# Kernel optimization log

Hardware: AMD Instinct MI355X
Metric: run time of the kernel (lower is better)

Reference implementation:

```python
import jax, jax.numpy as jnp
import numpy as np

N = 300_000      # active voxels
L = 128          # occupied bounding grid side
M = 32           # unet width m
CIN = 3          # input_feature_number
NCLASS = 20
K = 27           # 3x3x3 submanifold kernel
BLOCK_REPS = 2
BN_EPS = 1e-4


def _build_neighbors(rng):
    """Rulebook: for each active voxel, index of each of its 27 neighbors (N = missing)."""
    coords = rng.integers(0, L, size=(int(N * 1.5), 3), dtype=np.int64)
    keys = coords[:, 0] * L * L + coords[:, 1] * L + coords[:, 2]
    keys = np.unique(keys)[:N]
    assert keys.shape[0] == N
    x = keys // (L * L); y = (keys // L) % L; z = keys % L
    c = np.stack([x, y, z], 1)                      # [N,3] sorted-by-key coords
    nbr = np.full((N, K), N, dtype=np.int32)
    k = 0
    for dx in (-1, 0, 1):
        for dy in (-1, 0, 1):
            for dz in (-1, 0, 1):
                nc = c + np.array([dx, dy, dz])
                valid = ((nc >= 0) & (nc < L)).all(1)
                nk = nc[:, 0] * L * L + nc[:, 1] * L + nc[:, 2]
                pos = np.searchsorted(keys, nk).clip(0, N - 1)
                found = valid & (keys[pos] == nk)
                nbr[:, k] = np.where(found, pos, N).astype(np.int32)
                k += 1
    return nbr


def setup_inputs() -> dict:
    rng = np.random.default_rng(0)
    nbr_idx = jnp.asarray(_build_neighbors(rng))
    key = jax.random.key(0)
    ks = jax.random.split(key, 16)
    s = 0.1
    inp = {
        "features": jax.random.normal(ks[0], (N, CIN), jnp.float32),
        "nbr_idx": nbr_idx,
        # initial SubmanifoldConvolution(3, m, 3, bias=False)
        "w0": jax.random.normal(ks[1], (K, CIN, M), jnp.float32) * s,
        # residual tower params: [rep, conv_in_block(2), ...]
        "bw": jax.random.normal(ks[2], (BLOCK_REPS, 2, K, M, M), jnp.float32) * s,
        "bg": jnp.ones((BLOCK_REPS, 2, M), jnp.float32),
        "bb": jnp.zeros((BLOCK_REPS, 2, M), jnp.float32),
        # final BatchNormReLU(m)
        "gf": jnp.ones((M,), jnp.float32),
        "bf": jnp.zeros((M,), jnp.float32),
        # dense heads
        "w_cls": jax.random.normal(ks[3], (M, NCLASS), jnp.float32) * s,
        "b_cls": jnp.zeros((NCLASS,), jnp.float32),
        "w_fe": jax.random.normal(ks[4], (M, M), jnp.float32) * s,
        "b_fe": jnp.zeros((M,), jnp.float32),
        "w_le": jax.random.normal(ks[5], (M, M), jnp.float32) * s,
        "b_le": jnp.zeros((M,), jnp.float32),
        "w_fr": jax.random.normal(ks[6], (M, M), jnp.float32) * s,
        "b_fr": jnp.zeros((M,), jnp.float32),
        "w_lr": jax.random.normal(ks[7], (M, 1), jnp.float32) * s,
        "b_lr": jnp.zeros((1,), jnp.float32),
    }
    return inp


def _subconv(feat, nbr, W):
    # feat [N,Cin], nbr [N,27] with sentinel N -> zero row, W [27,Cin,Cout]
    fpad = jnp.concatenate([feat, jnp.zeros((1, feat.shape[1]), feat.dtype)], 0)
    gathered = fpad[nbr]                       # [N,27,Cin] irregular gather
    return jnp.einsum('nkc,kcd->nd', gathered, W)


def _bn(x, g, b):
    mu = x.mean(0)
    var = ((x - mu) ** 2).mean(0)
    return (x - mu) * jax.lax.rsqrt(var + BN_EPS) * g + b


def reference(features, nbr_idx, w0, bw, bg, bb, gf, bf,
              w_cls, b_cls, w_fe, b_fe, w_le, b_le, w_fr, b_fr, w_lr, b_lr):
    feat = _subconv(features, nbr_idx, w0)     # [N,M]
    for r in range(BLOCK_REPS):                # pre-activation residual blocks
        h = _subconv(jax.nn.relu(_bn(feat, bg[r, 0], bb[r, 0])), nbr_idx, bw[r, 0])
        h = _subconv(jax.nn.relu(_bn(h, bg[r, 1], bb[r, 1])), nbr_idx, bw[r, 1])
        feat = feat + h
    feat = jax.nn.relu(_bn(feat, gf, bf))      # BatchNormReLU(m) + OutputLayer
    y = feat @ w_cls + b_cls                                   # [N,20]
    embedding = (feat @ w_fe + b_fe) @ w_le + b_le             # [N,32]
    offset = jax.nn.sigmoid((feat @ w_fr + b_fr) @ w_lr + b_lr)  # [N,1]
    return (y, embedding, offset)
```

## Files before the change

### kernel.cpp

```cpp
#include <hip/hip_runtime.h>

#define NVOX 300000
#define K27 27
#define VPB 128
#define TILES 2
#define NBLK 2344
#define CPX  (NBLK/8)

typedef __attribute__((ext_vector_type(8))) __bf16 bf16x8;
typedef __attribute__((ext_vector_type(8))) unsigned short ushort8;
typedef __attribute__((ext_vector_type(4))) float f32x4;

__device__ inline unsigned short f2bf(float x){
  unsigned int u = __float_as_uint(x);
  unsigned int r = (u + 0x7FFFu + ((u >> 16) & 1u)) >> 16;
  return (unsigned short)r;
}

__global__ void pack_w_kernel(const float* __restrict__ bw, const float* __restrict__ w0,
                              unsigned short* __restrict__ pw, unsigned short* __restrict__ pw0){
  int t = blockIdx.x*256 + threadIdx.x;
  if (t < 4*K27*2*64){
    int l  = t & 63;
    int h  = (t >> 6) & 1;
    int k  = (t >> 7) % K27;
    int cv = t / (128*K27);
    int g = l >> 4, r16 = l & 15;
    ushort8 o;
    #pragma unroll
    for (int i = 0; i < 8; ++i){
      int c  = g*8 + i;
      int oc = h*16 + r16;
      o[i] = f2bf(bw[(((cv*K27 + k)*32) + c)*32 + oc]);
    }
    *reinterpret_cast<ushort8*>(pw + t*8) = o;
    return;
  }
  int u = t - 4*K27*2*64;
  if (u >= 4*2*64) return;
  int l  = u & 63;
  int h  = (u >> 6) & 1;
  int kb = u >> 7;
  int g = l >> 4, r16 = l & 15;
  int col = h*16 + r16;
  ushort8 o;
  #pragma unroll
  for (int i = 0; i < 8; ++i){
    int k   = kb*32 + g*8 + i;
    int tap = k >> 2, ch = k & 3;
    float v = (tap < K27 && ch < 3) ? w0[(tap*3 + ch)*32 + col] : 0.f;
    o[i] = f2bf(v);
  }
  *reinterpret_cast<ushort8*>(pw0 + u*8) = o;
}

__global__ void pack_hw_kernel(const float* __restrict__ w_cls, const float* __restrict__ b_cls,
                               const float* __restrict__ w_fe,  const float* __restrict__ b_fe,
                               const float* __restrict__ w_le,
                               const float* __restrict__ w_fr,  const float* __restrict__ b_fr,
                               unsigned short* __restrict__ pwh, float* __restrict__ bcat){
  int t = blockIdx.x*512 + threadIdx.x;
  if (t < 96){
    float v = 0.f;
    if (t < 32)      v = b_fe[t];
    else if (t < 64) v = b_fr[t-32];
    else if (t < 84) v = b_cls[t-64];
    bcat[t] = v;
  }
  if (t >= 8*64) return;
  int l = t & 63, f = t >> 6;
  int g = l >> 4, r16 = l & 15;
  ushort8 o;
  #pragma unroll
  for (int i = 0; i < 8; ++i){
    int k = g*8 + i;
    float v;
    if (f < 6){
      int col = f*16 + r16;
      if (col < 32)      v = w_fe[k*32 + col];
      else if (col < 64) v = w_fr[k*32 + (col-32)];
      else { int c = col - 64; v = (c < 20) ? w_cls[k*20 + c] : 0.f; }
    } else {
      int col = (f-6)*16 + r16;
      v = w_le[k*32 + col];
    }
    o[i] = f2bf(v);
  }
  *reinterpret_cast<ushort8*>(pwh + t*8) = o;
}

__global__ void prepad_kernel(const float* __restrict__ feats, f32x4* __restrict__ fpad){
  int row = blockIdx.x*256 + threadIdx.x;
  if (row > NVOX) return;
  f32x4 v = {0.f, 0.f, 0.f, 0.f};
  if (row < NVOX){
    v.x = feats[row*3+0]; v.y = feats[row*3+1]; v.z = feats[row*3+2];
  }
  fpad[row] = v;
}

__global__ void __launch_bounds__(256) conv0_mfma_kernel(
    const f32x4* __restrict__ fpad, const int* __restrict__ nbr,
    const unsigned short* __restrict__ pw0, float* __restrict__ trunk,
    float* __restrict__ stats){
  __shared__ int   snbr[256*K27];
  __shared__ float sstat[64];
  int tid  = threadIdx.x;
  int base = blockIdx.x*256;
  for (int i = tid; i < 256*K27; i += 256){
    int v = base + i / K27;
    snbr[i] = (v < NVOX) ? nbr[(size_t)base*K27 + i] : NVOX;
  }
  if (tid < 64) sstat[tid] = 0.f;
  __syncthreads();

  int l = tid & 63, w = tid >> 6;
  int g = l >> 4, r16 = l & 15;
  const int vb = w*64;

  bf16x8 B[4][2];
  #pragma unroll
  for (int kb = 0; kb < 4; ++kb)
    #pragma unroll
    for (int h = 0; h < 2; ++h)
      B[kb][h] = *reinterpret_cast<const bf16x8*>(pw0 + (kb*2 + h)*512 + l*8);

  f32x4 acc[4][2];
  #pragma unroll
  for (int t = 0; t < 4; ++t)
    #pragma unroll
    for (int h = 0; h < 2; ++h)
      acc[t][h] = (f32x4){0.f,0.f,0.f,0.f};

  #pragma unroll
  for (int t = 0; t < 4; ++t){
    int row = (vb + t*16 + r16)*K27;
    #pragma unroll
    for (int kb = 0; kb < 4; ++kb){
      int tap0 = kb*8 + g*2;
      int tap1 = tap0 + 1;
      int i0 = (tap0 < K27) ? tap0 : 0;
      int i1 = (tap1 < K27) ? tap1 : 0;
      int j0 = snbr[row + i0]; if (tap0 >= K27) j0 = NVOX;
      int j1 = snbr[row + i1]; if (tap1 >= K27) j1 = NVOX;
      f32x4 v0 = fpad[j0];
      f32x4 v1 = fpad[j1];
      ushort8 au;
      au[0] = f2bf(v0.x); au[1] = f2bf(v0.y); au[2] = f2bf(v0.z); au[3] = 0;
      au[4] = f2bf(v1.x); au[5] = f2bf(v1.y); au[6] = f2bf(v1.z); au[7] = 0;
      bf16x8 a = __builtin_bit_cast(bf16x8, au);
      acc[t][0] = __builtin_amdgcn_mfma_f32_16x16x32_bf16(a, B[kb][0], acc[t][0], 0, 0, 0);
      acc[t][1] = __builtin_amdgcn_mfma_f32_16x16x32_bf16(a, B[kb][1], acc[t][1], 0, 0, 0);
    }
  }

  float s0[2] = {0.f, 0.f}, s1[2] = {0.f, 0.f};
  #pragma unroll
  for (int t = 0; t < 4; ++t){
    #pragma unroll
    for (int r = 0; r < 4; ++r){
      int row = base + vb + t*16 + g*4 + r;
      if (row < NVOX){
        #pragma unroll
        for (int h = 0; h < 2; ++h){
          float v = acc[t][h][r];
          trunk[(size_t)row*32 + h*16 + r16] = v;
          s0[h] += v; s1[h] += v*v;
        }
      }
    }
  }
  #pragma unroll
  for (int h = 0; h < 2; ++h){
    s0[h] += __shfl_xor(s0[h], 16);
    s0[h] += __shfl_xor(s0[h], 32);
    s1[h] += __shfl_xor(s1[h], 16);
    s1[h] += __shfl_xor(s1[h], 32);
  }
  if (l < 16){
    atomicAdd(&sstat[r16],      s0[0]);
    atomicAdd(&sstat[32 + r16], s1[0]);
    atomicAdd(&sstat[16 + r16], s0[1]);
    atomicAdd(&sstat[48 + r16], s1[1]);
  }
  __syncthreads();
  if (tid < 64) atomicAdd(&stats[(blockIdx.x & 63)*64 + tid], sstat[tid]);
}

__global__ void __launch_bounds__(256) act_kernel(
    const float* __restrict__ trunk, const float* __restrict__ stats,
    const float* __restrict__ g, const float* __restrict__ b,
    unsigned short* __restrict__ act){
  __shared__ float sbnp[64];
  int tid = threadIdx.x;
  if (tid < 32){
    float s = 0.f, q = 0.f;
    #pragma unroll
    for (int i = 0; i < 64; ++i){ s += stats[i*64 + tid]; q += stats[i*64 + 32 + tid]; }
    float inv = 1.0f / (float)NVOX;
    float mu  = s * inv;
    float var = q * inv - mu*mu;
    float sc  = g[tid] * rsqrtf(var + 1e-4f);
    sbnp[tid]      = sc;
    sbnp[32 + tid] = b[tid] - mu*sc;
  }
  __syncthreads();

  int t = blockIdx.x*256 + tid;
  if (t >= (NVOX+1)*4) return;
  int row = t >> 2, part = t & 3;
  ushort8 o;
  if (row < NVOX){
    const float* p = trunk + (size_t)row*32 + part*8;
    #pragma unroll
    for (int i = 0; i < 8; ++i){
      float v = p[i]*sbnp[part*8 + i] + sbnp[32 + part*8 + i];
      v = fmaxf(v, 0.f);
      o[i] = f2bf(v);
    }
  } else {
    #pragma unroll
    for (int i = 0; i < 8; ++i) o[i] = 0;
  }
  *reinterpret_cast<ushort8*>(act + (size_t)row*32 + part*8) = o;
}

template<bool RES>
__global__ void __launch_bounds__(256) conv_mfma_kernel(
    const unsigned short* __restrict__ act, const int* __restrict__ nbr,
    const unsigned short* __restrict__ pw, float* __restrict__ trunk,
    float* __restrict__ stats){
  int bid   = blockIdx.x;
  int chunk = (bid & 7)*CPX + (bid >> 3);
  const int base = chunk*VPB;

  __shared__ int   snbr[VPB*K27];
  __shared__ float sstat[64];
  int tid = threadIdx.x;
  for (int i = tid; i < VPB*K27; i += 256){
    int v = base + i / K27;
    snbr[i] = (v < NVOX) ? nbr[(size_t)base*K27 + i] : NVOX;
  }
  if (tid < 64) sstat[tid] = 0.f;
  __syncthreads();

  int l = tid & 63, w = tid >> 6;
  int g = l >> 4, r16 = l & 15;
  const int vb = w*(TILES*16);

  int rb[TILES];
  #pragma unroll
  for (int t = 0; t < TILES; ++t) rb[t] = (vb + t*16 + r16)*K27;

  f32x4 acc[TILES][2];
  #pragma unroll
  for (int t = 0; t < TILES; ++t)
    #pragma unroll
    for (int h = 0; h < 2; ++h)
      acc[t][h] = (f32x4){0.f,0.f,0.f,0.f};

  #pragma unroll
  for (int k = 0; k < K27; ++k){
    bf16x8 b0 = *reinterpret_cast<const bf16x8*>(pw + (k*2    )*512 + l*8);
    bf16x8 b1 = *reinterpret_cast<const bf16x8*>(pw + (k*2 + 1)*512 + l*8);
    bf16x8 a[TILES];
    #pragma unroll
    for (int t = 0; t < TILES; ++t){
      int j = snbr[rb[t] + k];
      a[t] = *reinterpret_cast<const bf16x8*>(act + (size_t)j*32 + g*8);
    }
    #pragma unroll
    for (int t = 0; t < TILES; ++t){
      acc[t][0] = __builtin_amdgcn_mfma_f32_16x16x32_bf16(a[t], b0, acc[t][0], 0, 0, 0);
      acc[t][1] = __builtin_amdgcn_mfma_f32_16x16x32_bf16(a[t], b1, acc[t][1], 0, 0, 0);
    }
  }

  float s0[2] = {0.f, 0.f}, s1[2] = {0.f, 0.f};
  #pragma unroll
  for (int t = 0; t < TILES; ++t){
    #pragma unroll
    for (int r = 0; r < 4; ++r){
      int row = base + vb + t*16 + g*4 + r;
      if (row < NVOX){
        #pragma unroll
        for (int h = 0; h < 2; ++h){
          float v = acc[t][h][r];
          float* p = trunk + (size_t)row*32 + h*16 + r16;
          if (RES) v += *p;
          *p = v;
          s0[h] += v; s1[h] += v*v;
        }
      }
    }
  }
  #pragma unroll
  for (int h = 0; h < 2; ++h){
    s0[h] += __shfl_xor(s0[h], 16);
    s0[h] += __shfl_xor(s0[h], 32);
    s1[h] += __shfl_xor(s1[h], 16);
    s1[h] += __shfl_xor(s1[h], 32);
  }
  if (l < 16){
    atomicAdd(&sstat[r16],      s0[0]);
    atomicAdd(&sstat[32 + r16], s1[0]);
    atomicAdd(&sstat[16 + r16], s0[1]);
    atomicAdd(&sstat[48 + r16], s1[1]);
  }
  __syncthreads();
  if (tid < 64) atomicAdd(&stats[(blockIdx.x & 63)*64 + tid], sstat[tid]);
}

__global__ void __launch_bounds__(256) heads_mfma_kernel(
    const float* __restrict__ trunk, const float* __restrict__ stats,
    const float* __restrict__ gf, const float* __restrict__ bf,
    const unsigned short* __restrict__ pwh, const float* __restrict__ bcat,
    const float* __restrict__ b_le, const float* __restrict__ w_lr, const float* __restrict__ b_lr,
    float* __restrict__ out){
  __shared__ float lds[4][16][33];
  __shared__ float sbnp[64];
  int tid = threadIdx.x;
  if (tid < 32){
    float s = 0.f, q = 0.f;
    #pragma unroll
    for (int i = 0; i < 64; ++i){ s += stats[i*64 + tid]; q += stats[i*64 + 32 + tid]; }
    float inv = 1.0f / (float)NVOX;
    float mu  = s * inv;
    float var = q * inv - mu*mu;
    float sc  = gf[tid] * rsqrtf(var + 1e-4f);
    sbnp[tid]      = sc;
    sbnp[32 + tid] = bf[tid] - mu*sc;
  }
  __syncthreads();

  int l = tid & 63, w = tid >> 6;
  int g = l >> 4, r16 = l & 15;
  int base = blockIdx.x*256 + w*64;

  bf16x8 B1[6], B2[2];
  #pragma unroll
  for (int f = 0; f < 6; ++f)
    B1[f] = *reinterpret_cast<const bf16x8*>(pwh + f*512 + l*8);
  #pragma unroll
  for (int h = 0; h < 2; ++h)
    B2[h] = *reinterpret_cast<const bf16x8*>(pwh + (6+h)*512 + l*8);

  float sc[8], bi[8];
  #pragma unroll
  for (int i = 0; i < 8; ++i){ sc[i] = sbnp[g*8 + i]; bi[i] = sbnp[32 + g*8 + i]; }
  float wlr0 = w_lr[r16], wlr1 = w_lr[16 + r16];
  float blr  = b_lr[0];
  float bc0  = bcat[r16],      bc1  = bcat[16 + r16];
  float bc2  = bcat[32 + r16], bc3  = bcat[48 + r16];
  float bc4  = bcat[64 + r16], bc5  = bcat[80 + r16];
  float ble0 = b_le[r16],      ble1 = b_le[16 + r16];

  float* out_e = out + (size_t)NVOX*20;
  float* out_o = out + (size_t)NVOX*52;

  for (int t = 0; t < 4; ++t){
    int arow = base + t*16 + r16;
    f32x4 fa = {0.f,0.f,0.f,0.f}, fb2 = {0.f,0.f,0.f,0.f};
    if (arow < NVOX){
      const f32x4* p = reinterpret_cast<const f32x4*>(trunk + (size_t)arow*32 + g*8);
      fa  = p[0];
      fb2 = p[1];
    }
    ushort8 au;
    au[0] = f2bf(fmaxf(fa.x*sc[0] + bi[0], 0.f));
    au[1] = f2bf(fmaxf(fa.y*sc[1] + bi[1], 0.f));
    au[2] = f2bf(fmaxf(fa.z*sc[2] + bi[2], 0.f));
    au[3] = f2bf(fmaxf(fa.w*sc[3] + bi[3], 0.f));
    au[4] = f2bf(fmaxf(fb2.x*sc[4] + bi[4], 0.f));
    au[5] = f2bf(fmaxf(fb2.y*sc[5] + bi[5], 0.f));
    au[6] = f2bf(fmaxf(fb2.z*sc[6] + bi[6], 0.f));
    au[7] = f2bf(fmaxf(fb2.w*sc[7] + bi[7], 0.f));
    bf16x8 a = __builtin_bit_cast(bf16x8, au);

    f32x4 acc[6];
    #pragma unroll
    for (int j = 0; j < 6; ++j){
      acc[j] = (f32x4){0.f,0.f,0.f,0.f};
      acc[j] = __builtin_amdgcn_mfma_f32_16x16x32_bf16(a, B1[j], acc[j], 0, 0, 0);
    }

    #pragma unroll
    for (int r = 0; r < 4; ++r){
      int orow = base + t*16 + g*4 + r;
      if (orow < NVOX){
        out[(size_t)orow*20 + r16] = acc[4][r] + bc4;
        if (r16 < 4)
          out[(size_t)orow*20 + 16 + r16] = acc[5][r] + bc5;
      }
    }

    float part[4];
    #pragma unroll
    for (int r = 0; r < 4; ++r)
      part[r] = (acc[2][r] + bc2)*wlr0 + (acc[3][r] + bc3)*wlr1;
    #pragma unroll
    for (int r = 0; r < 4; ++r){
      part[r] += __shfl_xor(part[r], 1);
      part[r] += __shfl_xor(part[r], 2);
      part[r] += __shfl_xor(part[r], 4);
      part[r] += __shfl_xor(part[r], 8);
    }
    if (r16 == 0){
      #pragma unroll
      for (int r = 0; r < 4; ++r){
        int orow = base + t*16 + g*4 + r;
        if (orow < NVOX)
          out_o[orow] = 1.f/(1.f + __expf(-(part[r] + blr)));
      }
    }

    #pragma unroll
    for (int r = 0; r < 4; ++r){
      lds[w][g*4 + r][r16]      = acc[0][r] + bc0;
      lds[w][g*4 + r][16 + r16] = acc[1][r] + bc1;
    }
    ushort8 a2u;
    #pragma unroll
    for (int i = 0; i < 8; ++i)
      a2u[i] = f2bf(lds[w][r16][g*8 + i]);
    bf16x8 a2 = __builtin_bit_cast(bf16x8, a2u);
    f32x4 e0 = (f32x4){0.f,0.f,0.f,0.f}, e1 = (f32x4){0.f,0.f,0.f,0.f};
    e0 = __builtin_amdgcn_mfma_f32_16x16x32_bf16(a2, B2[0], e0, 0, 0, 0);
    e1 = __builtin_amdgcn_mfma_f32_16x16x32_bf16(a2, B2[1], e1, 0, 0, 0);
    #pragma unroll
    for (int r = 0; r < 4; ++r){
      int orow = base + t*16 + g*4 + r;
      if (orow < NVOX){
        out_e[(size_t)orow*32 + r16]      = e0[r] + ble0;
        out_e[(size_t)orow*32 + 16 + r16] = e1[r] + ble1;
      }
    }
  }
}

extern "C" void kernel_launch(void* const* d_in, const int* in_sizes, int n_in,
                              void* d_out, int out_size, void* d_ws, size_t ws_size,
                              hipStream_t stream){
  const float* features = (const float*)d_in[0];
  const int*   nbr      = (const int*)  d_in[1];
  const float* w0       = (const float*)d_in[2];
  const float* bw       = (const float*)d_in[3];
  const float* bg       = (const float*)d_in[4];
  const float* bb       = (const float*)d_in[5];
  const float* gf       = (const float*)d_in[6];
  const float* bf       = (const float*)d_in[7];
  const float* w_cls    = (const float*)d_in[8];
  const float* b_cls    = (const float*)d_in[9];
  const float* w_fe     = (const float*)d_in[10];
  const float* b_fe     = (const float*)d_in[11];
  const float* w_le     = (const float*)d_in[12];
  const float* b_le     = (const float*)d_in[13];
  const float* w_fr     = (const float*)d_in[14];
  const float* b_fr     = (const float*)d_in[15];
  const float* w_lr     = (const float*)d_in[16];
  const float* b_lr     = (const float*)d_in[17];
  float* out = (float*)d_out;

  char* ws = (char*)d_ws;
  float*          trunkA = (float*)(ws);
  float*          trunkH = (float*)(ws + 38400000);
  f32x4*          fpad   = (f32x4*)(ws + 38400000);
  unsigned short* actB   = (unsigned short*)(ws + 76800000);
  unsigned short* pw     = (unsigned short*)(ws + 96000128);
  unsigned short* pw0    = (unsigned short*)(ws + 96221312);
  float*          stats  = (float*)(ws + 96229504);
  unsigned short* pwh    = (unsigned short*)(ws + 96311424);
  float*          bcat   = (float*)(ws + 96319616);

  hipMemsetAsync(stats, 0, 5*64*64*sizeof(float), stream);
  pack_w_kernel<<<(4*K27*2*64 + 4*2*64 + 255)/256, 256, 0, stream>>>(bw, w0, pw, pw0);
  pack_hw_kernel<<<1, 512, 0, stream>>>(w_cls, b_cls, w_fe, b_fe, w_le, w_fr, b_fr, pwh, bcat);
  prepad_kernel<<<(NVOX + 256)/256, 256, 0, stream>>>(features, fpad);

  const int NB  = (NVOX + 255)/256;
  const int NA  = ((NVOX+1)*4 + 255)/256;

  conv0_mfma_kernel<<<NB, 256, 0, stream>>>(fpad, nbr, pw0, trunkA, stats + 0*4096);
  act_kernel<<<NA, 256, 0, stream>>>(trunkA, stats + 0*4096, bg +  0, bb +  0, actB);
  conv_mfma_kernel<false><<<NBLK, 256, 0, stream>>>(actB, nbr, pw + 0*27648, trunkH, stats + 1*4096);
  act_kernel<<<NA, 256, 0, stream>>>(trunkH, stats + 1*4096, bg + 32, bb + 32, actB);
  conv_mfma_kernel<true ><<<NBLK, 256, 0, stream>>>(actB, nbr, pw + 1*27648, trunkA, stats + 2*4096);
  act_kernel<<<NA, 256, 0, stream>>>(trunkA, stats + 2*4096, bg + 64, bb + 64, actB);
  conv_mfma_kernel<false><<<NBLK, 256, 0, stream>>>(actB, nbr, pw + 2*27648, trunkH, stats + 3*4096);
  act_kernel<<<NA, 256, 0, stream>>>(trunkH, stats + 3*4096, bg + 96, bb + 96, actB);
  conv_mfma_kernel<true ><<<NBLK, 256, 0, stream>>>(actB, nbr, pw + 3*27648, trunkA, stats + 4*4096);
  heads_mfma_kernel<<<NB, 256, 0, stream>>>(trunkA, stats + 4*4096, gf, bf, pwh, bcat,
                                            b_le, w_lr, b_lr, out);
}
```

Before: 450.7 us.

## Split conv K-loop across two wave groups with LDS reduction

The conv kernel now runs 512 threads per block. Two halves of the waves each process a disjoint subset of the 27 kernel offsets for the same voxel tiles. The second half writes its partial accumulators to shared memory, and the first half adds them before the store and statistics pass. This is meant to add more waves in flight to hide the latency of the irregular gathers, at the cost of extra shared memory (16 KB), a barrier, and half the waves sitting idle during the epilogue.

```diff
diff --git a/kernel.cpp b/kernel.cpp
--- a/kernel.cpp
+++ b/kernel.cpp
@@ -226,7 +226,7 @@
 }
 
 template<bool RES>
-__global__ void __launch_bounds__(256) conv_mfma_kernel(
+__global__ void __launch_bounds__(512) conv_mfma_kernel(
     const unsigned short* __restrict__ act, const int* __restrict__ nbr,
     const unsigned short* __restrict__ pw, float* __restrict__ trunk,
     float* __restrict__ stats){
@@ -235,9 +235,10 @@
   const int base = chunk*VPB;
 
   __shared__ int   snbr[VPB*K27];
+  __shared__ float sacc[16][4][64];
   __shared__ float sstat[64];
   int tid = threadIdx.x;
-  for (int i = tid; i < VPB*K27; i += 256){
+  for (int i = tid; i < VPB*K27; i += 512){
     int v = base + i / K27;
     snbr[i] = (v < NVOX) ? nbr[(size_t)base*K27 + i] : NVOX;
   }
@@ -245,12 +246,12 @@
   __syncthreads();
 
   int l = tid & 63, w = tid >> 6;
+  int vw = w & 3, half = w >> 2;
   int g = l >> 4, r16 = l & 15;
-  const int vb = w*(TILES*16);
-
-  int rb[TILES];
-  #pragma unroll
-  for (int t = 0; t < TILES; ++t) rb[t] = (vb + t*16 + r16)*K27;
+  const int vb = vw*(TILES*16);
+
+  const int rb0 = (vb      + r16)*K27;
+  const int rb1 = (vb + 16 + r16)*K27;
 
   f32x4 acc[TILES][2];
   #pragma unroll
@@ -259,53 +260,78 @@
     for (int h = 0; h < 2; ++h)
       acc[t][h] = (f32x4){0.f,0.f,0.f,0.f};
 
-  #pragma unroll
-  for (int k = 0; k < K27; ++k){
-    bf16x8 b0 = *reinterpret_cast<const bf16x8*>(pw + (k*2    )*512 + l*8);
-    bf16x8 b1 = *reinterpret_cast<const bf16x8*>(pw + (k*2 + 1)*512 + l*8);
-    bf16x8 a[TILES];
+#define KSTEP(kk) { \
+    bf16x8 b0 = *reinterpret_cast<const bf16x8*>(pw + ((kk)*2    )*512 + l*8); \
+    bf16x8 b1 = *reinterpret_cast<const bf16x8*>(pw + ((kk)*2 + 1)*512 + l*8); \
+    int j0 = snbr[rb0 + (kk)], j1 = snbr[rb1 + (kk)]; \
+    bf16x8 a0 = *reinterpret_cast<const bf16x8*>(act + (size_t)j0*32 + g*8); \
+    bf16x8 a1 = *reinterpret_cast<const bf16x8*>(act + (size_t)j1*32 + g*8); \
+    acc[0][0] = __builtin_amdgcn_mfma_f32_16x16x32_bf16(a0, b0, acc[0][0], 0, 0, 0); \
+    acc[0][1] = __builtin_amdgcn_mfma_f32_16x16x32_bf16(a0, b1, acc[0][1], 0, 0, 0); \
+    acc[1][0] = __builtin_amdgcn_mfma_f32_16x16x32_bf16(a1, b0, acc[1][0], 0, 0, 0); \
+    acc[1][1] = __builtin_amdgcn_mfma_f32_16x16x32_bf16(a1, b1, acc[1][1], 0, 0, 0); \
+  }
+
+  if (half == 0){
+    #pragma unroll
+    for (int k = 0; k < 14; ++k) KSTEP(k)
+  } else {
+    #pragma unroll
+    for (int k = 14; k < K27; ++k) KSTEP(k)
+  }
+#undef KSTEP
+
+  if (half == 1){
+    #pragma unroll
+    for (int t = 0; t < TILES; ++t)
+      #pragma unroll
+      for (int h = 0; h < 2; ++h)
+        #pragma unroll
+        for (int r = 0; r < 4; ++r)
+          sacc[t*8 + h*4 + r][vw][l] = acc[t][h][r];
+  }
+  __syncthreads();
+
+  if (half == 0){
+    #pragma unroll
+    for (int t = 0; t < TILES; ++t)
+      #pragma unroll
+      for (int h = 0; h < 2; ++h)
+        #pragma unroll
+        for (int r = 0; r < 4; ++r)
+          acc[t][h][r] += sacc[t*8 + h*4 + r][vw][l];
+
+    float s0[2] = {0.f, 0.f}, s1[2] = {0.f, 0.f};
     #pragma unroll
     for (int t = 0; t < TILES; ++t){
-      int j = snbr[rb[t] + k];
-      a[t] = *reinterpret_cast<const bf16x8*>(act + (size_t)j*32 + g*8);
-    }
-    #pragma unroll
-    for (int t = 0; t < TILES; ++t){
-      acc[t][0] = __builtin_amdgcn_mfma_f32_16x16x32_bf16(a[t], b0, acc[t][0], 0, 0, 0);
-      acc[t][1] = __builtin_amdgcn_mfma_f32_16x16x32_bf16(a[t], b1, acc[t][1], 0, 0, 0);
-    }
-  }
-
-  float s0[2] = {0.f, 0.f}, s1[2] = {0.f, 0.f};
-  #pragma unroll
-  for (int t = 0; t < TILES; ++t){
-    #pragma unroll
-    for (int r = 0; r < 4; ++r){
-      int row = base + vb + t*16 + g*4 + r;
-      if (row < NVOX){
-        #pragma unroll
-        for (int h = 0; h < 2; ++h){
-          float v = acc[t][h][r];
-          float* p = trunk + (size_t)row*32 + h*16 + r16;
-          if (RES) v += *p;
-          *p = v;
-          s0[h] += v; s1[h] += v*v;
+      #pragma unroll
+      for (int r = 0; r < 4; ++r){
+        int row = base + vb + t*16 + g*4 + r;
+        if (row < NVOX){
+          #pragma unroll
+          for (int h = 0; h < 2; ++h){
+            float v = acc[t][h][r];
+            float* p = trunk + (size_t)row*32 + h*16 + r16;
+            if (RES) v += *p;
+            *p = v;
+            s0[h] += v; s1[h] += v*v;
+          }
         }
       }
     }
-  }
-  #pragma unroll
-  for (int h = 0; h < 2; ++h){
-    s0[h] += __shfl_xor(s0[h], 16);
-    s0[h] += __shfl_xor(s0[h], 32);
-    s1[h] += __shfl_xor(s1[h], 16);
-    s1[h] += __shfl_xor(s1[h], 32);
-  }
-  if (l < 16){
-    atomicAdd(&sstat[r16],      s0[0]);
-    atomicAdd(&sstat[32 + r16], s1[0]);
-    atomicAdd(&sstat[16 + r16], s0[1]);
-    atomicAdd(&sstat[48 + r16], s1[1]);
+    #pragma unroll
+    for (int h = 0; h < 2; ++h){
+      s0[h] += __shfl_xor(s0[h], 16);
+      s0[h] += __shfl_xor(s0[h], 32);
+      s1[h] += __shfl_xor(s1[h], 16);
+      s1[h] += __shfl_xor(s1[h], 32);
+    }
+    if (l < 16){
+      atomicAdd(&sstat[r16],      s0[0]);
+      atomicAdd(&sstat[32 + r16], s1[0]);
+      atomicAdd(&sstat[16 + r16], s0[1]);
+      atomicAdd(&sstat[48 + r16], s1[1]);
+    }
   }
   __syncthreads();
   if (tid < 64) atomicAdd(&stats[(blockIdx.x & 63)*64 + tid], sstat[tid]);
@@ -482,13 +508,13 @@
 
   conv0_mfma_kernel<<<NB, 256, 0, stream>>>(fpad, nbr, pw0, trunkA, stats + 0*4096);
   act_kernel<<<NA, 256, 0, stream>>>(trunkA, stats + 0*4096, bg +  0, bb +  0, actB);
-  conv_mfma_kernel<false><<<NBLK, 256, 0, stream>>>(actB, nbr, pw + 0*27648, trunkH, stats + 1*4096);
+  conv_mfma_kernel<false><<<NBLK, 512, 0, stream>>>(actB, nbr, pw + 0*27648, trunkH, stats + 1*4096);
   act_kernel<<<NA, 256, 0, stream>>>(trunkH, stats + 1*4096, bg + 32, bb + 32, actB);
-  conv_mfma_kernel<true ><<<NBLK, 256, 0, stream>>>(actB, nbr, pw + 1*27648, trunkA, stats + 2*4096);
+  conv_mfma_kernel<true ><<<NBLK, 512, 0, stream>>>(actB, nbr, pw + 1*27648, trunkA, stats + 2*4096);
   act_kernel<<<NA, 256, 0, stream>>>(trunkA, stats + 2*4096, bg + 64, bb + 64, actB);
-  conv_mfma_kernel<false><<<NBLK, 256, 0, stream>>>(actB, nbr, pw + 2*27648, trunkH, stats + 3*4096);
+  conv_mfma_kernel<false><<<NBLK, 512, 0, stream>>>(actB, nbr, pw + 2*27648, trunkH, stats + 3*4096);
   act_kernel<<<NA, 256, 0, stream>>>(trunkH, stats + 3*4096, bg + 96, bb + 96, actB);
-  conv_mfma_kernel<true ><<<NBLK, 256, 0, stream>>>(actB, nbr, pw + 3*27648, trunkA, stats + 4*4096);
+  conv_mfma_kernel<true ><<<NBLK, 512, 0, stream>>>(actB, nbr, pw + 3*27648, trunkA, stats + 4*4096);
   heads_mfma_kernel<<<NB, 256, 0, stream>>>(trunkA, stats + 4*4096, gf, bf, pwh, bcat,
                                             b_le, w_lr, b_lr, out);
 }
```

New measurement: 444.8 us. About the same (-1.3%).
